# Optimization experiments

Measured on AMD Instinct MI355X. Metric: run time of the kernel, lower is better.

Reference implementation:

```python
import jax, jax.numpy as jnp
import numpy as np

B, S, E, H, T, V = 32, 512, 256, 512, 8, 32000
G = 4 * H  # gate width


def setup_inputs() -> dict:
    key = jax.random.key(0)
    ks = jax.random.split(key, 14)
    s = 0.02  # init scale to keep tanh/sigmoid out of saturation
    return {
        "x": jax.random.randint(ks[0], (B, S), 0, V),
        "TASK": 0,
        "embed": jax.random.normal(ks[1], (V, E), jnp.float32) * s,
        "Wx_t": jax.random.normal(ks[2], (T, E, G), jnp.float32) * s,
        "Wh_t": jax.random.normal(ks[3], (T, H, G), jnp.float32) * s,
        "b_t": jnp.zeros((T, G), jnp.float32),
        "Ws_p1": jax.random.normal(ks[4], (H, H), jnp.float32) * s,
        "Ws_p2": jax.random.normal(ks[5], (H + E, H), jnp.float32) * s,
        "Us_w": jax.random.normal(ks[6], (H, 1), jnp.float32) * s,
        "Us_b": jnp.zeros((1,), jnp.float32),
        "Wx_c": jax.random.normal(ks[7], (E, G), jnp.float32) * s,
        "Wh_c": jax.random.normal(ks[8], (H, G), jnp.float32) * s,
        "Wm_c": jax.random.normal(ks[9], (H, G), jnp.float32) * s,
        "b_c": jnp.zeros((G,), jnp.float32),
    }


def _lstm_cell(g, c):
    i, f, gg, o = jnp.split(g, 4, axis=-1)
    c_new = jax.nn.sigmoid(f) * c + jax.nn.sigmoid(i) * jnp.tanh(gg)
    h_new = jax.nn.sigmoid(o) * jnp.tanh(c_new)
    return h_new, c_new


def _task_messages(emb, Wx, Wh, b):
    # emb [B,S,E]; Wx [K,E,4H]; returns aggregated messages [S,B,H,K]
    K = Wx.shape[0]
    xg = jnp.einsum('bse,keg->skbg', emb, Wx)  # precompute input gates [S,K,B,4H]
    h0 = jnp.zeros((K, emb.shape[0], Wh.shape[1]), emb.dtype)

    def step(carry, xg_t):
        h, c = carry  # [K,B,H]
        g = xg_t + jnp.einsum('kbh,khg->kbg', h, Wh) + b[:, None, :]
        h, c = _lstm_cell(g, c)
        return (h, c), h

    _, hs = jax.lax.scan(step, (h0, h0), xg)  # hs [S,K,B,H]
    return jnp.transpose(hs, (0, 2, 3, 1))  # [S,B,H,K]


def reference(x, TASK, embed, Wx_t, Wh_t, b_t, Ws_p1, Ws_p2, Us_w, Us_b,
              Wx_c, Wh_c, Wm_c, b_c):
    emb = embed[x]  # [B,S,E]
    other = np.array([i for i in range(Wx_t.shape[0]) if i != TASK])
    agg = _task_messages(emb, Wx_t[other], Wh_t[other], b_t[other])  # [S,B,H,K]

    emb_s = jnp.swapaxes(emb, 0, 1)          # [S,B,E]
    xg_c = emb_s @ Wx_c                       # [S,B,4H] precomputed input gates
    Bsz, Hdim = x.shape[0], Wh_c.shape[0]
    h0 = jnp.zeros((Bsz, Hdim), emb.dtype)

    def step(carry, inp):
        h, c = carry
        agg_t, emb_t, xg_t = inp  # [B,H,K], [B,E], [B,4H]
        # attention over the K task messages
        v1 = jnp.einsum('ij,bjk->bik', Ws_p1, agg_t) \
             + (jnp.concatenate([h, emb_t], axis=-1) @ Ws_p2)[:, :, None]
        v2 = jnp.tanh(v1)                                  # [B,H,K]
        Si = jnp.einsum('bhk,ho->bk', v2, Us_w) + Us_b     # [B,K]
        a = jax.nn.softmax(Si, axis=1)
        Rt = jnp.einsum('bk,bhk->bh', a, agg_t)            # [B,H]
        # custom LSTM cell step with message input Rt
        g = xg_t + h @ Wh_c + Rt @ Wm_c + b_c
        h, c = _lstm_cell(g, c)
        return (h, c), h

    (hN, cN), outs = jax.lax.scan(step, (h0, h0), (agg, emb_s, xg_c))
    out = jnp.swapaxes(outs, 0, 1)  # [B,S,H]
    return out, hN
```

## Files before the change

### kernel.cpp

```cpp
#include <hip/hip_runtime.h>

#define S_ 512
#define SCOPE __HIP_MEMORY_SCOPE_AGENT

typedef short bf16x8 __attribute__((ext_vector_type(8)));
typedef float f32x4 __attribute__((ext_vector_type(4)));

__device__ __forceinline__ float sigm(float x) { return 1.f / (1.f + expf(-x)); }
__device__ __forceinline__ float b2f(unsigned short u) {
    return __builtin_bit_cast(float, (unsigned)u << 16);
}
__device__ __forceinline__ unsigned short f2b(float f) {
    unsigned x = __builtin_bit_cast(unsigned, f);
    return (unsigned short)((x + 0x7fffu + ((x >> 16) & 1u)) >> 16);
}
__device__ __forceinline__ float ldcf(const float* p) {
    return __hip_atomic_load(p, __ATOMIC_RELAXED, SCOPE);
}
__device__ __forceinline__ unsigned ldc32(const void* p) {
    return __hip_atomic_load((const unsigned*)p, __ATOMIC_RELAXED, SCOPE);
}
__device__ __forceinline__ unsigned long long ldc64(const void* p) {
    return __hip_atomic_load((const unsigned long long*)p, __ATOMIC_RELAXED, SCOPE);
}
__device__ __forceinline__ void stg32(void* p, unsigned v) {
    __hip_atomic_store((unsigned*)p, v, __ATOMIC_RELAXED, SCOPE);
}
__device__ __forceinline__ void stgf(float* p, float v) {
    __hip_atomic_store(p, v, __ATOMIC_RELAXED, SCOPE);
}
__device__ __forceinline__ bf16x8 frag_c(const unsigned short* p) {
    union { unsigned long long q[2]; bf16x8 v; } u;
    u.q[0] = ldc64(p); u.q[1] = ldc64(p + 4);
    return u.v;
}
__device__ __forceinline__ bf16x8 frag_p(const unsigned short* p) {
    return *(const bf16x8*)p;
}

__device__ __forceinline__ void gbar(unsigned* bar, int tid, int wg, unsigned n) {
    __syncthreads();
    if (tid == 0) {
        int g = wg >> 5;
        unsigned* gcnt = bar + 64 + g * 32;
        unsigned* ggen = bar + 320 + g * 32;
        unsigned old = __hip_atomic_fetch_add(gcnt, 1u, __ATOMIC_RELAXED, SCOPE);
        if (old == n * 32u - 1u) {
            unsigned rold = __hip_atomic_fetch_add(bar, 1u, __ATOMIC_RELAXED, SCOPE);
            if (rold == n * 8u - 1u) {
                __hip_atomic_store(bar + 32, n, __ATOMIC_RELAXED, SCOPE);
            } else {
                while (__hip_atomic_load(bar + 32, __ATOMIC_RELAXED, SCOPE) < n)
                    __builtin_amdgcn_s_sleep(1);
            }
            __hip_atomic_store(ggen, n, __ATOMIC_RELAXED, SCOPE);
        } else {
            while (__hip_atomic_load(ggen, __ATOMIC_RELAXED, SCOPE) < n)
                __builtin_amdgcn_s_sleep(1);
        }
        asm volatile("" ::: "memory");
    }
    __syncthreads();
}

__global__ __launch_bounds__(512) void fused_all(
        const int* __restrict__ x, const int* __restrict__ taskp,
        const float* __restrict__ embed,
        const float* __restrict__ Wx_t, const float* __restrict__ Wh_t,
        const float* __restrict__ b_t,
        const float* __restrict__ Ws_p1, const float* __restrict__ Ws_p2,
        const float* __restrict__ Us_w,
        const float* __restrict__ Wx_c, const float* __restrict__ Wh_c,
        const float* __restrict__ Wm_c, const float* __restrict__ b_c,
        float* __restrict__ out,
        unsigned short* __restrict__ WTa,  unsigned short* __restrict__ WTp2,
        unsigned short* __restrict__ WTp1, unsigned short* __restrict__ WTc,
        unsigned short* __restrict__ embbf, unsigned short* __restrict__ hbf,
        unsigned short* __restrict__ hmbf,
        float* __restrict__ ctask, float* __restrict__ cmain,
        float* __restrict__ p2w, float* __restrict__ partial,
        float* __restrict__ hNf, unsigned* __restrict__ bar)
{
    __shared__ float smem[8320];
    __shared__ unsigned short swA[64 * 776];
    const int wg = blockIdx.x, tid = threadIdx.x;
    const int lane = tid & 63, wave = tid >> 6;
    const int rowm = lane & 15, ks = lane >> 4;
    const int task = taskp[0];
    unsigned bn = 0;

    for (int i = wg * 512 + tid; i < 114688; i += 131072) stg32((unsigned*)hbf + i, 0u);
    for (int i = wg * 512 + tid; i < 16384; i += 131072) stg32((unsigned*)hmbf + i, 0u);
    for (int i = wg * 512 + tid; i < 114688; i += 131072) stgf(ctask + i, 0.f);
    for (int i = wg * 512 + tid; i < 16384; i += 131072) stgf(cmain + i, 0.f);
    for (int i = wg * 512 + tid; i < 2097152; i += 131072) {
        int ts = i >> 12, b = (i >> 7) & 31, ep = i & 127;
        int tok = x[b * S_ + ts];
        const float* s = embed + (size_t)tok * 256 + 2 * ep;
        stg32((unsigned*)embbf + i, (unsigned)f2b(s[0]) | ((unsigned)f2b(s[1]) << 16));
    }
    for (int i = wg * 512 + tid; i < 5505024; i += 131072) {
        int s = i / 24576, r = i % 24576, kp = r >> 6, cg = r & 63;
        int k = s >> 5, nt = s & 31, kk = k + (k >= task);
        int col = ((cg >> 4) << 9) + nt * 16 + (cg & 15);
        int kr = kp * 2;
        const float* src = (kr < 256)
            ? Wx_t + (size_t)kk * 524288 + (size_t)kr * 2048 + col
            : Wh_t + (size_t)kk * 1048576 + (size_t)(kr - 256) * 2048 + col;
        stg32((unsigned*)WTa + (size_t)s * 24576 + cg * 384 + kp,
              (unsigned)f2b(src[0]) | ((unsigned)f2b(src[2048]) << 16));
    }
    for (int i = wg * 512 + tid; i < 196608; i += 131072) {
        int p = i / 24576, r = i % 24576, kp = r >> 6, cg = r & 63;
        int col = p * 64 + cg, kr = kp * 2;
        const float* src = Ws_p2 + (size_t)kr * 512 + col;
        stg32((unsigned*)WTp2 + p * 24576 + cg * 384 + kp,
              (unsigned)f2b(src[0]) | ((unsigned)f2b(src[512]) << 16));
    }
    for (int i = wg * 512 + tid; i < 131072; i += 131072) {
        const float* src = Ws_p1 + 2 * (size_t)i;
        stg32((unsigned*)WTp1 + i, (unsigned)f2b(src[0]) | ((unsigned)f2b(src[1]) << 16));
    }
    for (int i = wg * 512 + tid; i < 1310720; i += 131072) {
        int ntc = i / 10240, r = i % 10240, kp = r >> 4, cg = r & 15;
        int col = ((cg >> 2) << 9) + ntc * 4 + (cg & 3);
        int kr = kp * 2;
        const float* src = (kr < 256) ? Wx_c + (size_t)kr * 2048 + col
                         : (kr < 768) ? Wh_c + (size_t)(kr - 256) * 2048 + col
                                      : Wm_c + (size_t)(kr - 768) * 2048 + col;
        stg32((unsigned*)WTc + ntc * 10240 + cg * 640 + kp,
              (unsigned)f2b(src[0]) | ((unsigned)f2b(src[2048]) << 16));
    }
    gbar(bar, tid, wg, ++bn);

    if (wg < 232) {
        const unsigned* srcw = (const unsigned*)(wg < 224
            ? WTa + (size_t)wg * 49152 : WTp2 + (size_t)(wg - 224) * 49152);
        for (int i = tid; i < 24576; i += 512) {
            int cg = i / 384, kp = i % 384;
            ((unsigned*)(swA + cg * 776))[kp] = srcw[cg * 384 + kp];
        }
    }
    __syncthreads();

    const int xq = wg & 7, jq = wg >> 3;
    const int kB = jq >> 2, itB = xq + 8 * (jq & 3);

    for (int t = 0; t < S_; ++t) {
        const int old = t & 1, nw = old ^ 1;
        const unsigned short* hb_old = hbf + old * 114688;
        unsigned short* hb_new = hbf + nw * 114688;
        const unsigned short* hm_old = hmbf + old * 16384;
        unsigned short* hm_new = hmbf + nw * 16384;
        const unsigned short* et = embbf + (size_t)t * 8192;

        if (wg < 232) {
            const bool istask = wg < 224;
            unsigned short* sh = (unsigned short*)smem;
            const unsigned short* hsrc = istask ? hb_old + (wg >> 5) * 16384 : hm_old;
            for (int i = tid; i < 4096; i += 512) {
                int row = i >> 7, c8 = i & 127;
                *(unsigned long long*)(sh + row * 520 + c8 * 4) =
                    ldc64(hsrc + row * 512 + c8 * 4);
            }
            __syncthreads();
            f32x4 acc = {0.f, 0.f, 0.f, 0.f};
            if (istask) {
                int k = wg >> 5, nt = wg & 31;
                int mt = wave >> 2, g = wave & 3;
                int b = mt * 16 + rowm;
                const unsigned short* wtp = swA + (g * 16 + rowm) * 776;
                const unsigned short* ep_ = et + b * 256;
                const unsigned short* shb = sh + b * 520;
#pragma unroll
                for (int kt = 0; kt < 24; ++kt) {
                    int ko = kt * 32 + ks * 8;
                    bf16x8 bf = frag_p(wtp + ko);
                    bf16x8 af = (kt < 8) ? frag_p(ep_ + ko) : frag_p(shb + ko - 256);
                    acc = __builtin_amdgcn_mfma_f32_16x16x32_bf16(af, bf, acc, 0, 0, 0);
                }
                __syncthreads();
                float* sg = smem;
#pragma unroll
                for (int r2 = 0; r2 < 4; ++r2)
                    sg[(mt * 16 + (lane >> 4) * 4 + r2) * 64 + g * 16 + rowm] = acc[r2];
                __syncthreads();
                {
                    int b2 = tid >> 4, hc = tid & 15;
                    int kk = k + (k >= task);
                    const float* bb = b_t + kk * 2048 + nt * 16 + hc;
                    float gi = sg[b2 * 64 + hc]      + bb[0];
                    float gf = sg[b2 * 64 + 16 + hc] + bb[512];
                    float gg = sg[b2 * 64 + 32 + hc] + bb[1024];
                    float go = sg[b2 * 64 + 48 + hc] + bb[1536];
                    int cidx = (k * 32 + b2) * 512 + nt * 16 + hc;
                    float cold = ctask[cidx];
                    float cn = sigm(gf) * cold + sigm(gi) * tanhf(gg);
                    float hn = sigm(go) * tanhf(cn);
                    ctask[cidx] = cn;
                    int hbits = (int)f2b(hn);
                    int oth = __shfl_xor(hbits, 1, 64);
                    if ((hc & 1) == 0)
                        stg32(hb_new + cidx, (unsigned)hbits | ((unsigned)oth << 16));
                }
            } else {
                int pb = wg - 224;
                int mt = wave >> 2, q = wave & 3;
                int b = mt * 16 + rowm;
                int cg = q * 16 + rowm;
                const unsigned short* wtp = swA + cg * 776;
                const unsigned short* ep_ = et + b * 256;
                const unsigned short* shb = sh + b * 520;
#pragma unroll
                for (int kt = 0; kt < 24; ++kt) {
                    int ko = kt * 32 + ks * 8;
                    bf16x8 bf = frag_p(wtp + ko);
                    bf16x8 af = (kt < 16) ? frag_p(shb + ko) : frag_p(ep_ + ko - 512);
                    acc = __builtin_amdgcn_mfma_f32_16x16x32_bf16(af, bf, acc, 0, 0, 0);
                }
#pragma unroll
                for (int r2 = 0; r2 < 4; ++r2)
                    stgf(p2w + (mt * 16 + (lane >> 4) * 4 + r2) * 512 + pb * 64 + cg, acc[r2]);
            }
        }
        gbar(bar, tid, wg, ++bn);

        if (wg < 224) {
            int mt = wave & 1, kq = wave >> 1;
            f32x4 acc = {0.f, 0.f, 0.f, 0.f};
            const unsigned short* wtp = WTp1 + (itB * 16 + rowm) * 512;
            const unsigned short* hp_ = hb_new + (kB * 32 + mt * 16 + rowm) * 512;
#pragma unroll
            for (int s4 = 0; s4 < 4; ++s4) {
                int ko = (kq * 4 + s4) * 32 + ks * 8;
                bf16x8 bf = frag_p(wtp + ko);
                bf16x8 af = frag_c(hp_ + ko);
                acc = __builtin_amdgcn_mfma_f32_16x16x32_bf16(af, bf, acc, 0, 0, 0);
            }
            ((f32x4*)smem)[wave * 64 + lane] = acc;
            __syncthreads();
            {
                int b2 = tid >> 4, i2 = tid & 15;
                int mt2 = b2 >> 4, rr = b2 & 15;
                int ln = ((rr & 12) << 2) | i2, rg = rr & 3;
                float val = 0.f;
#pragma unroll
                for (int q2 = 0; q2 < 4; ++q2)
                    val += smem[((q2 * 2 + mt2) * 64 + ln) * 4 + rg];
                val += ldcf(p2w + b2 * 512 + itB * 16 + i2);
                float sv = tanhf(val) * Us_w[itB * 16 + i2];
                sv += __shfl_xor(sv, 1, 64); sv += __shfl_xor(sv, 2, 64);
                sv += __shfl_xor(sv, 4, 64); sv += __shfl_xor(sv, 8, 64);
                if (i2 == 0) stgf(partial + (kB * 32 + itB) * 32 + b2, sv);
            }
        }
        gbar(bar, tid, wg, ++bn);

        {
            int mh = wg >> 7, ntc = wg & 127;
            unsigned short* Rt = (unsigned short*)smem;
            float* sredc = smem + 4160;
            float* ssi = smem + 6208;
            float* sa  = smem + 6320;
            float* sg2 = smem + 6432;
            float* sred4 = smem + 6688;
            if (tid < 448) {
                int kq = tid % 7, bl = (tid / 7) % 16, part = tid / 112;
                const float* pp = partial + (size_t)kq * 1024 + (size_t)(part * 8) * 32
                                + mh * 16 + bl;
                float v0 = ldcf(pp);        float v1 = ldcf(pp + 32);
                float v2 = ldcf(pp + 64);   float v3 = ldcf(pp + 96);
                float v4 = ldcf(pp + 128);  float v5 = ldcf(pp + 160);
                float v6 = ldcf(pp + 192);  float v7 = ldcf(pp + 224);
                sred4[part * 112 + bl * 7 + kq] =
                    ((v0 + v1) + (v2 + v3)) + ((v4 + v5) + (v6 + v7));
            }
            __syncthreads();
            if (tid < 112)
                ssi[tid] = (sred4[tid] + sred4[112 + tid])
                         + (sred4[224 + tid] + sred4[336 + tid]);
            __syncthreads();
            if (tid < 16) {
                float mx = -1e30f;
                for (int kq = 0; kq < 7; ++kq) mx = fmaxf(mx, ssi[tid * 7 + kq]);
                float den = 0.f, e[7];
                for (int kq = 0; kq < 7; ++kq) { e[kq] = expf(ssi[tid * 7 + kq] - mx); den += e[kq]; }
                float rd = 1.f / den;
                for (int kq = 0; kq < 7; ++kq) sa[tid * 7 + kq] = e[kq] * rd;
            }
            __syncthreads();
            for (int i = tid; i < 4096; i += 512) {
                int bl = i >> 8, rp = i & 255;
                const unsigned short* hb0 = hb_new + (mh * 16 + bl) * 512 + 2 * rp;
                unsigned u0 = ldc32(hb0);
                unsigned u1 = ldc32(hb0 + 16384);
                unsigned u2 = ldc32(hb0 + 32768);
                unsigned u3 = ldc32(hb0 + 49152);
                unsigned u4 = ldc32(hb0 + 65536);
                unsigned u5 = ldc32(hb0 + 81920);
                unsigned u6 = ldc32(hb0 + 98304);
                const float* sab = sa + bl * 7;
                float a0 = 0.f, a1 = 0.f;
                a0 = fmaf(sab[0], b2f((unsigned short)u0), a0);
                a1 = fmaf(sab[0], b2f((unsigned short)(u0 >> 16)), a1);
                a0 = fmaf(sab[1], b2f((unsigned short)u1), a0);
                a1 = fmaf(sab[1], b2f((unsigned short)(u1 >> 16)), a1);
                a0 = fmaf(sab[2], b2f((unsigned short)u2), a0);
                a1 = fmaf(sab[2], b2f((unsigned short)(u2 >> 16)), a1);
                a0 = fmaf(sab[3], b2f((unsigned short)u3), a0);
                a1 = fmaf(sab[3], b2f((unsigned short)(u3 >> 16)), a1);
                a0 = fmaf(sab[4], b2f((unsigned short)u4), a0);
                a1 = fmaf(sab[4], b2f((unsigned short)(u4 >> 16)), a1);
                a0 = fmaf(sab[5], b2f((unsigned short)u5), a0);
                a1 = fmaf(sab[5], b2f((unsigned short)(u5 >> 16)), a1);
                a0 = fmaf(sab[6], b2f((unsigned short)u6), a0);
                a1 = fmaf(sab[6], b2f((unsigned short)(u6 >> 16)), a1);
                Rt[bl * 520 + 2 * rp]     = f2b(a0);
                Rt[bl * 520 + 2 * rp + 1] = f2b(a1);
            }
            __syncthreads();
            f32x4 acc = {0.f, 0.f, 0.f, 0.f};
            const unsigned short* wtp = WTc + (size_t)ntc * 20480 + rowm * 1280;
            int b = mh * 16 + rowm;
            const unsigned short* ep_ = et + b * 256;
            const unsigned short* hp_ = hm_old + b * 512;
            const unsigned short* rp_ = Rt + rowm * 520;
#pragma unroll
            for (int s5 = 0; s5 < 5; ++s5) {
                int kt = wave * 5 + s5;
                int ko = kt * 32 + ks * 8;
                bf16x8 bf = frag_p(wtp + ko);
                bf16x8 af;
                if (kt < 8) af = frag_p(ep_ + ko);
                else if (kt < 24) af = frag_c(hp_ + ko - 256);
                else af = frag_p(rp_ + ko - 768);
                acc = __builtin_amdgcn_mfma_f32_16x16x32_bf16(af, bf, acc, 0, 0, 0);
            }
            __syncthreads();
            ((f32x4*)sredc)[wave * 64 + lane] = acc;
            __syncthreads();
            if (tid < 256) {
                int rr = tid >> 4, c = tid & 15;
                int ln = ((rr & 12) << 2) | c, rg = rr & 3;
                float val = 0.f;
#pragma unroll
                for (int w2 = 0; w2 < 8; ++w2) val += sredc[(w2 * 64 + ln) * 4 + rg];
                sg2[rr * 16 + c] = val;
            }
            __syncthreads();
            if (tid < 64) {
                int bl = tid >> 2, j = tid & 3;
                int b2 = mh * 16 + bl;
                int colh = ntc * 4 + j;
                float gi = sg2[bl * 16 + 0  + j] + b_c[colh];
                float gf = sg2[bl * 16 + 4  + j] + b_c[512 + colh];
                float gg = sg2[bl * 16 + 8  + j] + b_c[1024 + colh];
                float go = sg2[bl * 16 + 12 + j] + b_c[1536 + colh];
                int cidx = b2 * 512 + colh;
                float cold = cmain[cidx];
                float cn = sigm(gf) * cold + sigm(gi) * tanhf(gg);
                float hn = sigm(go) * tanhf(cn);
                cmain[cidx] = cn;
                out[(size_t)b2 * 262144 + (size_t)t * 512 + colh] = hn;
                int hbits = (int)f2b(hn);
                int oth = __shfl_xor(hbits, 1, 64);
                if ((j & 1) == 0)
                    stg32(hm_new + cidx, (unsigned)hbits | ((unsigned)oth << 16));
                if (t == 511) stgf(hNf + cidx, hn);
            }
        }
        gbar(bar, tid, wg, ++bn);
    }

    for (int i = wg * 512 + tid; i < 16384; i += 131072)
        out[8388608 + i] = ldcf(hNf + i);
}

extern "C" void kernel_launch(void* const* d_in, const int* in_sizes, int n_in,
                              void* d_out, int out_size, void* d_ws, size_t ws_size,
                              hipStream_t stream) {
    const int*   x      = (const int*)d_in[0];
    const int*   taskp  = (const int*)d_in[1];
    const float* embed  = (const float*)d_in[2];
    const float* Wx_t   = (const float*)d_in[3];
    const float* Wh_t   = (const float*)d_in[4];
    const float* b_t    = (const float*)d_in[5];
    const float* Ws_p1  = (const float*)d_in[6];
    const float* Ws_p2  = (const float*)d_in[7];
    const float* Us_w   = (const float*)d_in[8];
    const float* Wx_c   = (const float*)d_in[10];
    const float* Wh_c   = (const float*)d_in[11];
    const float* Wm_c   = (const float*)d_in[12];
    const float* b_c    = (const float*)d_in[13];
    float* out = (float*)d_out;

    unsigned short* us = (unsigned short*)d_ws;
    unsigned short* WTa   = us;
    unsigned short* WTp2  = WTa   + 11010048;
    unsigned short* WTp1  = WTp2  + 393216;
    unsigned short* WTc   = WTp1  + 262144;
    unsigned short* embbf = WTc   + 2621440;
    unsigned short* hbf   = embbf + 4194304;
    unsigned short* hmbf  = hbf   + 229376;
    float* fb      = (float*)(hmbf + 32768);
    float* ctask   = fb;
    float* cmain   = ctask + 114688;
    float* p2w     = cmain + 16384;
    float* partial = p2w   + 16384;
    float* hNf     = partial + 7168;
    unsigned* bar  = (unsigned*)(hNf + 16384);

    hipMemsetAsync(bar, 0, 4096, stream);

    void* args[] = { (void*)&x, (void*)&taskp, (void*)&embed,
                     (void*)&Wx_t, (void*)&Wh_t, (void*)&b_t,
                     (void*)&Ws_p1, (void*)&Ws_p2, (void*)&Us_w,
                     (void*)&Wx_c, (void*)&Wh_c, (void*)&Wm_c, (void*)&b_c,
                     (void*)&out,
                     (void*)&WTa, (void*)&WTp2, (void*)&WTp1, (void*)&WTc,
                     (void*)&embbf, (void*)&hbf, (void*)&hmbf,
                     (void*)&ctask, (void*)&cmain, (void*)&p2w, (void*)&partial,
                     (void*)&hNf, (void*)&bar };
    hipLaunchCooperativeKernel((void*)fused_all, dim3(256), dim3(512), args, 0, stream);
}
```

Before: 10.55 ms.

## Replace per-phase grid barriers with fine-grained dependency counters

Swaps the three grid-wide barriers per timestep for per-group atomic counters. Each phase bumps a counter when it finishes and spins only on the specific producers it depends on, so work groups can run ahead of unrelated stages. The partial-score buffer is double-buffered by timestep parity to avoid write-after-read hazards across steps. This adds the risk of subtle ordering bugs, since the counters use relaxed and release atomics without matching acquire loads, and it needs more workspace.

```diff
diff --git a/kernel.cpp b/kernel.cpp
--- a/kernel.cpp
+++ b/kernel.cpp
@@ -61,6 +61,15 @@
         asm volatile("" ::: "memory");
     }
     __syncthreads();
+}
+
+#define CNT(i) (bar + 1024 + (i) * 32)
+__device__ __forceinline__ void spin_ge(unsigned* p, unsigned thr) {
+    while (__hip_atomic_load(p, __ATOMIC_RELAXED, SCOPE) < thr)
+        __builtin_amdgcn_s_sleep(1);
+}
+__device__ __forceinline__ void bump(unsigned* p) {
+    __hip_atomic_fetch_add(p, 1u, __ATOMIC_RELEASE, SCOPE);
 }
 
 __global__ __launch_bounds__(512) void fused_all(
@@ -87,7 +96,6 @@
     const int lane = tid & 63, wave = tid >> 6;
     const int rowm = lane & 15, ks = lane >> 4;
     const int task = taskp[0];
-    unsigned bn = 0;
 
     for (int i = wg * 512 + tid; i < 114688; i += 131072) stg32((unsigned*)hbf + i, 0u);
     for (int i = wg * 512 + tid; i < 16384; i += 131072) stg32((unsigned*)hmbf + i, 0u);
@@ -131,7 +139,7 @@
         stg32((unsigned*)WTc + ntc * 10240 + cg * 640 + kp,
               (unsigned)f2b(src[0]) | ((unsigned)f2b(src[2048]) << 16));
     }
-    gbar(bar, tid, wg, ++bn);
+    gbar(bar, tid, wg, 1);
 
     if (wg < 232) {
         const unsigned* srcw = (const unsigned*)(wg < 224
@@ -153,9 +161,17 @@
         const unsigned short* hm_old = hmbf + old * 16384;
         unsigned short* hm_new = hmbf + nw * 16384;
         const unsigned short* et = embbf + (size_t)t * 8192;
+        float* pbuf = partial + (t & 1) * 7168;
 
         if (wg < 232) {
             const bool istask = wg < 224;
+            {
+                unsigned* wp = nullptr; unsigned wthr = 0;
+                if (istask) { if (tid == 0) { wp = CNT(wg >> 5); wthr = 32u * t; } }
+                else if (tid < 8) { wp = CNT(15 + tid); wthr = 32u * t; }
+                if (wp) spin_ge(wp, wthr);
+            }
+            __syncthreads();
             unsigned short* sh = (unsigned short*)smem;
             const unsigned short* hsrc = istask ? hb_old + (wg >> 5) * 16384 : hm_old;
             for (int i = tid; i < 4096; i += 512) {
@@ -203,6 +219,8 @@
                     if ((hc & 1) == 0)
                         stg32(hb_new + cidx, (unsigned)hbits | ((unsigned)oth << 16));
                 }
+                __syncthreads();
+                if (tid == 0) bump(CNT(k));
             } else {
                 int pb = wg - 224;
                 int mt = wave >> 2, q = wave & 3;
@@ -221,11 +239,22 @@
 #pragma unroll
                 for (int r2 = 0; r2 < 4; ++r2)
                     stgf(p2w + (mt * 16 + (lane >> 4) * 4 + r2) * 512 + pb * 64 + cg, acc[r2]);
+                __syncthreads();
+                if (tid == 0) bump(CNT(7));
             }
         }
-        gbar(bar, tid, wg, ++bn);
 
         if (wg < 224) {
+            {
+                unsigned* wp = nullptr; unsigned wthr = 0;
+                if (tid == 0) { wp = CNT(kB); wthr = 32u * (t + 1); }
+                else if (tid == 1) { wp = CNT(7); wthr = 8u * (t + 1); }
+                else if (tid >= 2 && tid < 10 && t >= 1) {
+                    wp = CNT(15 + tid - 2); wthr = 32u * (t - 1);
+                }
+                if (wp) spin_ge(wp, wthr);
+            }
+            __syncthreads();
             int mt = wave & 1, kq = wave >> 1;
             f32x4 acc = {0.f, 0.f, 0.f, 0.f};
             const unsigned short* wtp = WTp1 + (itB * 16 + rowm) * 512;
@@ -251,12 +280,20 @@
                 float sv = tanhf(val) * Us_w[itB * 16 + i2];
                 sv += __shfl_xor(sv, 1, 64); sv += __shfl_xor(sv, 2, 64);
                 sv += __shfl_xor(sv, 4, 64); sv += __shfl_xor(sv, 8, 64);
-                if (i2 == 0) stgf(partial + (kB * 32 + itB) * 32 + b2, sv);
-            }
+                if (i2 == 0) stgf(pbuf + (kB * 32 + itB) * 32 + b2, sv);
+            }
+            __syncthreads();
+            if (tid == 0) bump(CNT(8 + kB));
         }
-        gbar(bar, tid, wg, ++bn);
 
         {
+            {
+                unsigned* wp = nullptr; unsigned wthr = 0;
+                if (tid < 7) { wp = CNT(8 + tid); wthr = 32u * (t + 1); }
+                else if (tid < 15) { wp = CNT(15 + tid - 7); wthr = 32u * t; }
+                if (wp) spin_ge(wp, wthr);
+            }
+            __syncthreads();
             int mh = wg >> 7, ntc = wg & 127;
             unsigned short* Rt = (unsigned short*)smem;
             float* sredc = smem + 4160;
@@ -266,7 +303,7 @@
             float* sred4 = smem + 6688;
             if (tid < 448) {
                 int kq = tid % 7, bl = (tid / 7) % 16, part = tid / 112;
-                const float* pp = partial + (size_t)kq * 1024 + (size_t)(part * 8) * 32
+                const float* pp = pbuf + (size_t)kq * 1024 + (size_t)(part * 8) * 32
                                 + mh * 16 + bl;
                 float v0 = ldcf(pp);        float v1 = ldcf(pp + 32);
                 float v2 = ldcf(pp + 64);   float v3 = ldcf(pp + 96);
@@ -368,10 +405,13 @@
                     stg32(hm_new + cidx, (unsigned)hbits | ((unsigned)oth << 16));
                 if (t == 511) stgf(hNf + cidx, hn);
             }
+            __syncthreads();
+            if (tid == 0) bump(CNT(15 + (wg >> 5)));
         }
-        gbar(bar, tid, wg, ++bn);
-    }
-
+    }
+
+    if (tid < 8) spin_ge(CNT(15 + tid), 32u * 512u);
+    __syncthreads();
     for (int i = wg * 512 + tid; i < 16384; i += 131072)
         out[8388608 + i] = ldcf(hNf + i);
 }
@@ -407,10 +447,10 @@
     float* cmain   = ctask + 114688;
     float* p2w     = cmain + 16384;
     float* partial = p2w   + 16384;
-    float* hNf     = partial + 7168;
+    float* hNf     = partial + 14336;
     unsigned* bar  = (unsigned*)(hNf + 16384);
 
-    hipMemsetAsync(bar, 0, 4096, stream);
+    hipMemsetAsync(bar, 0, 8192, stream);
 
     void* args[] = { (void*)&x, (void*)&taskp, (void*)&embed,
                      (void*)&Wx_t, (void*)&Wh_t, (void*)&b_t,
```

New measurement: 17.54 ms. 66.4% more time.
